# Optimization experiments

Measured on AMD Instinct MI355X. Metric: run time of the kernel, lower is better.

Reference implementation:

```python
import jax, jax.numpy as jnp
import numpy as np

P, N, E, H = 8192, 32, 256, 8
D = E // H
CUT_A, CUT_B = 0.001, 0.005  # self.length_range = (0.001, 0.005, None, None)
SQRT3 = 1.7320508075688772


def _soft_square_cutoff(x):
    # smooth ramp 0->1 on [CUT_A, CUT_B], 0 below, 1 above (high-side ranges are None)
    t = jnp.clip((x - CUT_A) / (CUT_B - CUT_A), 0.0, 1.0)
    return 0.5 * (1.0 - jnp.cos(jnp.pi * t))


def setup_inputs() -> dict:
    key = jax.random.key(0)
    ks = jax.random.split(key, 16)
    s = 1.0 / np.sqrt(E)
    inp = {
        "query": jax.random.normal(ks[0], (P, E), jnp.float32),
        "key_x": jax.random.normal(ks[1], (P, E), jnp.float32),
        "value": jax.random.normal(ks[2], (P, E), jnp.float32),
        "index_pair": jax.random.randint(ks[3], (P, N), 0, P),
        "relative_atten_weights": jax.random.normal(ks[4], (P, N, H), jnp.float32),
        # lengths ~ N(0, 0.002*sqrt(3)) so they span the (0.001, 0.005) cutoff range
        "rpe_distance": jax.random.normal(ks[5], (P, N, 3), jnp.float32) * 0.002,
        "Wq": jax.random.normal(ks[6], (E, E), jnp.float32) * s,
        "bq": jnp.zeros((E,), jnp.float32),
        "Wk": jax.random.normal(ks[7], (E, E), jnp.float32) * s,
        "bk": jnp.zeros((E,), jnp.float32),
        "Wv": jax.random.normal(ks[8], (E, E), jnp.float32) * s,
        "bv": jnp.zeros((E,), jnp.float32),
        "Wg1": jax.random.normal(ks[9], (E, 3 * H), jnp.float32) * s,
        "bg1": jnp.zeros((3 * H,), jnp.float32),
        "Wg2": jax.random.normal(ks[10], (3 * H, 3 * H), jnp.float32) * (1.0 / np.sqrt(3 * H)),
        "bg2": jnp.zeros((3 * H,), jnp.float32),
    }
    return inp


def reference(query, key_x, value, index_pair, relative_atten_weights, rpe_distance,
              Wq, bq, Wk, bk, Wv, bv, Wg1, bg1, Wg2, bg2):
    # --- RPE spherical harmonics (irreps 1x0e+1x1e, component norm); keep l=1 part ([:,1:])
    rlen = jnp.linalg.norm(rpe_distance, axis=-1, keepdims=True)        # [P,N,1]
    unit = rpe_distance / jnp.maximum(rlen, 1e-12)                      # normalize=True
    cutoff = _soft_square_cutoff(rlen)                                  # nonscalar cutoff
    rpe_edge_sh = SQRT3 * unit * cutoff                                 # [P,N,3]

    # --- projections
    q = query @ Wq + bq                                                 # [P,E]
    k = key_x @ Wk + bk
    v = value @ Wv + bv

    # --- mapper_v6: per-edge gather of key/value rows
    k_g = k[index_pair]                                                 # [P,N,E]
    v_g = v[index_pair]                                                 # [P,N,E]

    # --- dot-product attention logits
    qh = q.reshape(P, H, D)
    kh = k_g.reshape(P, N, H, D)
    dot_atten = jnp.einsum('phd,pnhd->pnh', qh, kh)                     # [P,N,H]

    # --- MLP positional bias gated by spherical harmonics
    diff = k_g - q[:, None, :]                                          # [P,N,E]
    g = jax.nn.relu(diff @ Wg1 + bg1) @ Wg2 + bg2                       # [P,N,3H]
    g = g.reshape(P, N, H, 3)
    pos_atten = jnp.sum(g * rpe_edge_sh[:, :, None, :], axis=-1)        # [P,N,H]

    atten = (dot_atten + pos_atten + relative_atten_weights) / np.sqrt(D)
    atten = jax.nn.softmax(atten, axis=1)                               # over neighbors

    vh = v_g.reshape(P, N, H, D)
    out = jnp.einsum('pnh,pnhc->phc', atten, vh).reshape(P, E)
    return out
```

## Files before the change

### kernel.cpp

```cpp
#include <hip/hip_runtime.h>
#include <stdint.h>

typedef uint32_t u32;
typedef unsigned short u16;

#define LDT 40

typedef __bf16 bf16x8 __attribute__((ext_vector_type(8)));
typedef float  f32x4  __attribute__((ext_vector_type(4)));

__device__ __forceinline__ float bf2f(u16 x) {
  union { float f; u32 u; } c; c.u = ((u32)x) << 16; return c.f;
}
__device__ __forceinline__ u16 f2bf(float f) {
  union { float f; u32 u; } c; c.f = f;
  u32 b = c.u;
  return (u16)((b + 0x7FFFu + ((b >> 16) & 1u)) >> 16);
}
__device__ __forceinline__ u32 pk2(float lo, float hi) {
  return (u32)f2bf(lo) | ((u32)f2bf(hi) << 16);
}

__global__ __launch_bounds__(256) void prep_transpose(
    const float* __restrict__ Wq, const float* __restrict__ Wk, const float* __restrict__ Wv,
    u16* __restrict__ WTq, u16* __restrict__ WTk, u16* __restrict__ WTv)
{
  int z = blockIdx.z, bx = blockIdx.x, by = blockIdx.y;
  int x = threadIdx.x, y = threadIdx.y;
  __shared__ u16 tile[32][33];
  const float* W  = (z == 0) ? Wq : (z == 1) ? Wk : Wv;
  u16*         WT = (z == 0) ? WTq : (z == 1) ? WTk : WTv;
  for (int yy = y; yy < 32; yy += 8)
    tile[yy][x] = f2bf(W[(size_t)(by * 32 + yy) * 256 + bx * 32 + x]);
  __syncthreads();
  for (int yy = y; yy < 32; yy += 8)
    WT[(size_t)(bx * 32 + yy) * 256 + by * 32 + x] = tile[x][yy];
}

__global__ __launch_bounds__(256) void prep_comb(
    const u16* __restrict__ WTq, const u16* __restrict__ WTk,
    const float* __restrict__ Wg1, const float* __restrict__ bg1,
    const float* __restrict__ bq, const float* __restrict__ bk,
    u16* __restrict__ CT, float* __restrict__ bcomb)
{
  int c = blockIdx.x, z = blockIdx.y;
  int t = threadIdx.x;
  const u16*   WT = (z == 0) ? WTq : WTk;
  const float* b  = (z == 0) ? bq : bk;

  float acc = 0.f;
#pragma unroll 8
  for (int e = 0; e < 256; e++)
    acc += bf2f(WT[(size_t)e * 256 + t]) * Wg1[(size_t)e * 24 + c];
  CT[(size_t)z * 8192 + (size_t)c * 256 + t] = f2bf(acc);

  __shared__ float red[256];
  red[t] = b[t] * Wg1[(size_t)t * 24 + c];
  __syncthreads();
  for (int s = 128; s > 0; s >>= 1) {
    if (t < s) red[t] += red[t + s];
    __syncthreads();
  }
  if (t == 0)
    bcomb[z * 24 + c] = red[0] - ((z == 0) ? bg1[c] : 0.f);
}

__global__ __launch_bounds__(256) void gemm_qkv(
    const float* __restrict__ Xq, const float* __restrict__ Xk, const float* __restrict__ Xv,
    const u16* __restrict__ WTq, const u16* __restrict__ WTk, const u16* __restrict__ WTv,
    const float* __restrict__ bq, const float* __restrict__ bk, const float* __restrict__ bv,
    const u16* __restrict__ CT, const float* __restrict__ bcomb,
    u16* __restrict__ Oq, u16* __restrict__ Ok, u16* __restrict__ Ov,
    float* __restrict__ qadj, float* __restrict__ kg1)
{
  int z = blockIdx.z;
  int nblk = blockIdx.x;
  if (nblk == 2 && z == 2) return;

  const float* X = (z == 0) ? Xq : (z == 1) ? Xk : Xv;
  int m0 = blockIdx.y * 128;
  int t = threadIdx.x;
  int lane = t & 63, wid = t >> 6;
  int fr = lane & 15, fg = lane >> 4;
  int sr = t >> 1;
  int sc = (t & 1) * 16;

  __shared__ __align__(16) u16 la[128 * LDT];
  __shared__ __align__(16) u16 lb[128 * LDT];

  if (nblk < 2) {
    const u16*   WT   = (z == 0) ? WTq : (z == 1) ? WTk : WTv;
    const float* bias = (z == 0) ? bq : (z == 1) ? bk : bv;
    u16*         O    = (z == 0) ? Oq : (z == 1) ? Ok : Ov;
    int n0 = nblk * 128;
    int wr = wid >> 1, wc = wid & 1;

    f32x4 acc[4][4];
#pragma unroll
    for (int i = 0; i < 4; i++)
#pragma unroll
      for (int j = 0; j < 4; j++) acc[i][j] = (f32x4){0.f, 0.f, 0.f, 0.f};

    for (int kt = 0; kt < 256; kt += 32) {
      const float4* ga = (const float4*)(X + (size_t)(m0 + sr) * 256 + kt + sc);
      float4 a0 = ga[0], a1 = ga[1], a2 = ga[2], a3 = ga[3];
      const uint4* gb = (const uint4*)(WT + (size_t)(n0 + sr) * 256 + kt + sc);
      uint4 b0 = gb[0], b1 = gb[1];

      uint4 wa0, wa1;
      wa0.x = pk2(a0.x, a0.y); wa0.y = pk2(a0.z, a0.w);
      wa0.z = pk2(a1.x, a1.y); wa0.w = pk2(a1.z, a1.w);
      wa1.x = pk2(a2.x, a2.y); wa1.y = pk2(a2.z, a2.w);
      wa1.z = pk2(a3.x, a3.y); wa1.w = pk2(a3.z, a3.w);

      __syncthreads();
      *(uint4*)&la[sr * LDT + sc]     = wa0;
      *(uint4*)&la[sr * LDT + sc + 8] = wa1;
      *(uint4*)&lb[sr * LDT + sc]     = b0;
      *(uint4*)&lb[sr * LDT + sc + 8] = b1;
      __syncthreads();

      bf16x8 af[4], bfr[4];
#pragma unroll
      for (int s = 0; s < 4; s++)
        af[s] = *(const bf16x8*)&la[(wr * 64 + s * 16 + fr) * LDT + fg * 8];
#pragma unroll
      for (int s = 0; s < 4; s++)
        bfr[s] = *(const bf16x8*)&lb[(wc * 64 + s * 16 + fr) * LDT + fg * 8];
#pragma unroll
      for (int i = 0; i < 4; i++)
#pragma unroll
        for (int j = 0; j < 4; j++)
          acc[i][j] = __builtin_amdgcn_mfma_f32_16x16x32_bf16(af[i], bfr[j], acc[i][j], 0, 0, 0);
    }

#pragma unroll
    for (int i = 0; i < 4; i++) {
      int rowb = m0 + wr * 64 + i * 16 + fg * 4;
#pragma unroll
      for (int j = 0; j < 4; j++) {
        int col = n0 + wc * 64 + j * 16 + fr;
        float bb = bias[col];
#pragma unroll
        for (int r = 0; r < 4; r++)
          O[(size_t)(rowb + r) * 256 + col] = f2bf(acc[i][j][r] + bb);
      }
    }
  } else {
    const u16*   BT = CT + (size_t)z * 8192;
    const float* bc = bcomb + z * 24;
    float*       O  = (z == 0) ? qadj : kg1;

    f32x4 acc[2][2];
#pragma unroll
    for (int i = 0; i < 2; i++)
#pragma unroll
      for (int j = 0; j < 2; j++) acc[i][j] = (f32x4){0.f, 0.f, 0.f, 0.f};

    for (int kt = 0; kt < 256; kt += 32) {
      const float4* ga = (const float4*)(X + (size_t)(m0 + sr) * 256 + kt + sc);
      float4 a0 = ga[0], a1 = ga[1], a2 = ga[2], a3 = ga[3];
      uint4 b0, b1;
      if (t < 64) {
        const uint4* gb = (const uint4*)(BT + (size_t)sr * 256 + kt + sc);
        b0 = gb[0]; b1 = gb[1];
      }
      uint4 wa0, wa1;
      wa0.x = pk2(a0.x, a0.y); wa0.y = pk2(a0.z, a0.w);
      wa0.z = pk2(a1.x, a1.y); wa0.w = pk2(a1.z, a1.w);
      wa1.x = pk2(a2.x, a2.y); wa1.y = pk2(a2.z, a2.w);
      wa1.z = pk2(a3.x, a3.y); wa1.w = pk2(a3.z, a3.w);

      __syncthreads();
      *(uint4*)&la[sr * LDT + sc]     = wa0;
      *(uint4*)&la[sr * LDT + sc + 8] = wa1;
      if (t < 64) {
        *(uint4*)&lb[sr * LDT + sc]     = b0;
        *(uint4*)&lb[sr * LDT + sc + 8] = b1;
      }
      __syncthreads();

      bf16x8 af[2], bfr[2];
#pragma unroll
      for (int s = 0; s < 2; s++)
        af[s] = *(const bf16x8*)&la[(wid * 32 + s * 16 + fr) * LDT + fg * 8];
#pragma unroll
      for (int s = 0; s < 2; s++)
        bfr[s] = *(const bf16x8*)&lb[(s * 16 + fr) * LDT + fg * 8];
#pragma unroll
      for (int i = 0; i < 2; i++)
#pragma unroll
        for (int j = 0; j < 2; j++)
          acc[i][j] = __builtin_amdgcn_mfma_f32_16x16x32_bf16(af[i], bfr[j], acc[i][j], 0, 0, 0);
    }

#pragma unroll
    for (int i = 0; i < 2; i++) {
      int rowb = m0 + wid * 32 + i * 16 + fg * 4;
#pragma unroll
      for (int j = 0; j < 2; j++) {
        int col = j * 16 + fr;
        if (col < 24) {
#pragma unroll
          for (int r = 0; r < 4; r++)
            O[(size_t)(rowb + r) * 24 + col] = acc[i][j][r] + bc[col];
        }
      }
    }
  }
}

__global__ __launch_bounds__(256) void attn_logits(
    const u16* __restrict__ qb, const u16* __restrict__ kb,
    const float* __restrict__ kg1, const float* __restrict__ qadj,
    const int* __restrict__ ip, const float* __restrict__ raw,
    const float* __restrict__ rpe, const float* __restrict__ wg2b,
    const float* __restrict__ bg2b, float* __restrict__ att)
{
  int p = blockIdx.x, t = threadIdx.x;
  __shared__ __align__(16) float q_s[256];
  __shared__            int   idx_s[32];
  __shared__            float rpe_s[96];
  __shared__            float sh_s[32][3];
  __shared__            float qadj_s[24];
  __shared__            float bg2_s[24];
  __shared__            float wg2_s[576];
  __shared__ __align__(16) float kg1_s[32 * 24];
  __shared__            float pre_s[32][24];
  __shared__            float logit_s[32][8];
  __shared__            float ps_s[64];
  __shared__            float is_s[8];

  q_s[t] = bf2f(qb[(size_t)p * 256 + t]);
  if (t < 96) rpe_s[t] = rpe[(size_t)p * 96 + t];
  if (t < 32) idx_s[t] = ip[(size_t)p * 32 + t];
  if (t >= 128 && t < 152) qadj_s[t - 128] = qadj[(size_t)p * 24 + (t - 128)];
  if (t >= 160 && t < 184) bg2_s[t - 160] = bg2b[t - 160];
  if (t < 192) {
    wg2_s[t]       = wg2b[t];
    wg2_s[t + 192] = wg2b[t + 192];
    wg2_s[t + 384] = wg2b[t + 384];
  }
  __syncthreads();

  if (t < 32) {
    float x  = rpe_s[t * 3 + 0];
    float y  = rpe_s[t * 3 + 1];
    float zz = rpe_s[t * 3 + 2];
    float rl = sqrtf(x * x + y * y + zz * zz);
    float inv = 1.f / fmaxf(rl, 1e-12f);
    float tt = (rl - 0.001f) * 250.f;
    tt = fminf(fmaxf(tt, 0.f), 1.f);
    float cut = 0.5f * (1.f - cosf(tt * 3.14159265358979f));
    float s3c = 1.7320508075688772f * inv * cut;
    sh_s[t][0] = x * s3c; sh_s[t][1] = y * s3c; sh_s[t][2] = zz * s3c;
  }
  if (t < 192) {
    int n = t / 6, f = t % 6;
    const float4* kp = (const float4*)(kg1 + (size_t)idx_s[n] * 24);
    *(float4*)&kg1_s[n * 24 + f * 4] = kp[f];
  }
  __syncthreads();

  {
    int n = t >> 3, jj = t & 7;
#pragma unroll
    for (int c = 0; c < 3; c++) {
      int i = jj * 3 + c;
      pre_s[n][i] = fmaxf(kg1_s[n * 24 + i] - qadj_s[i], 0.f);
    }
  }
  __syncthreads();

  {
    int n = t >> 3, h = t & 7;
    const uint4*  kr = (const uint4*)(kb + (size_t)idx_s[n] * 256 + h * 32);
    const float4* qr = (const float4*)(q_s + h * 32);
    float dot = 0.f;
#pragma unroll
    for (int c = 0; c < 4; c++) {
      uint4 kw = kr[c];
      float4 q0 = qr[2 * c], q1 = qr[2 * c + 1];
      dot += bf2f((u16)(kw.x & 0xFFFF)) * q0.x + bf2f((u16)(kw.x >> 16)) * q0.y;
      dot += bf2f((u16)(kw.y & 0xFFFF)) * q0.z + bf2f((u16)(kw.y >> 16)) * q0.w;
      dot += bf2f((u16)(kw.z & 0xFFFF)) * q1.x + bf2f((u16)(kw.z >> 16)) * q1.y;
      dot += bf2f((u16)(kw.w & 0xFFFF)) * q1.z + bf2f((u16)(kw.w >> 16)) * q1.w;
    }
    float g0 = bg2_s[h * 3 + 0], g1v = bg2_s[h * 3 + 1], g2v = bg2_s[h * 3 + 2];
#pragma unroll
    for (int i = 0; i < 24; i++) {
      float pr = pre_s[n][i];
      int b = i * 24 + h * 3;
      g0  += pr * wg2_s[b + 0];
      g1v += pr * wg2_s[b + 1];
      g2v += pr * wg2_s[b + 2];
    }
    float pos = g0 * sh_s[n][0] + g1v * sh_s[n][1] + g2v * sh_s[n][2];
    float rw = raw[(size_t)p * 256 + t];
    logit_s[n][h] = __expf((dot + pos + rw) * 0.17677669529663687f);
  }
  __syncthreads();

  if (t < 64) {
    int h = t & 7, g = t >> 3;
    float s = logit_s[g * 4 + 0][h] + logit_s[g * 4 + 1][h]
            + logit_s[g * 4 + 2][h] + logit_s[g * 4 + 3][h];
    ps_s[h * 8 + g] = s;
  }
  __syncthreads();
  if (t < 8) {
    float s = 0.f;
#pragma unroll
    for (int g = 0; g < 8; g++) s += ps_s[t * 8 + g];
    is_s[t] = 1.f / s;
  }
  __syncthreads();

  {
    int h = t >> 5, n = t & 31;
    att[(size_t)p * 256 + t] = logit_s[n][h] * is_s[h];
  }
}

__global__ __launch_bounds__(256) void attn_pv(
    const u16* __restrict__ vb, const float* __restrict__ att,
    const int* __restrict__ ip, float* __restrict__ out)
{
  int p0 = blockIdx.x * 4, t = threadIdx.x;
  int wid = t >> 6, l = t & 63;
  int p = p0 + wid;
  __shared__ __align__(16) float att_s[4][256];
  __shared__            int   idx_s[4][32];

  *(float4*)&att_s[wid][l * 4] = *(const float4*)(att + (size_t)p * 256 + l * 4);
  if (l < 32) idx_s[wid][l] = ip[(size_t)p * 32 + l];
  __syncthreads();

  int h = l >> 3;
  float a0 = 0.f, a1 = 0.f, a2 = 0.f, a3 = 0.f;
#pragma unroll
  for (int n = 0; n < 32; n++) {
    float w = att_s[wid][h * 32 + n];
    const uint2 vv = *(const uint2*)(vb + (size_t)idx_s[wid][n] * 256 + l * 4);
    a0 += w * bf2f((u16)(vv.x & 0xFFFF));
    a1 += w * bf2f((u16)(vv.x >> 16));
    a2 += w * bf2f((u16)(vv.y & 0xFFFF));
    a3 += w * bf2f((u16)(vv.y >> 16));
  }
  float4 r; r.x = a0; r.y = a1; r.z = a2; r.w = a3;
  *(float4*)(out + (size_t)p * 256 + l * 4) = r;
}

extern "C" void kernel_launch(void* const* d_in, const int* in_sizes, int n_in,
                              void* d_out, int out_size, void* d_ws, size_t ws_size,
                              hipStream_t stream) {
  const float* query = (const float*)d_in[0];
  const float* key_x = (const float*)d_in[1];
  const float* value = (const float*)d_in[2];
  const int*   index_pair = (const int*)d_in[3];
  const float* raw  = (const float*)d_in[4];
  const float* rpe  = (const float*)d_in[5];
  const float* Wq = (const float*)d_in[6];
  const float* bq = (const float*)d_in[7];
  const float* Wk = (const float*)d_in[8];
  const float* bk = (const float*)d_in[9];
  const float* Wv = (const float*)d_in[10];
  const float* bv = (const float*)d_in[11];
  const float* Wg1 = (const float*)d_in[12];
  const float* bg1 = (const float*)d_in[13];
  const float* Wg2 = (const float*)d_in[14];
  const float* bg2 = (const float*)d_in[15];
  float* out = (float*)d_out;

  char* ws = (char*)d_ws;
  u16*   qbuf = (u16*)(ws);
  u16*   kbuf = (u16*)(ws + (4u << 20));
  u16*   vbuf = (u16*)(ws + (8u << 20));
  float* att  = (float*)(ws + (12u << 20));
  float* qadj = (float*)(ws + (20u << 20));
  float* kg1  = (float*)(ws + (20u << 20) + 786432);
  u16*   WTq  = (u16*)(ws + (20u << 20) + 2 * 786432);
  u16*   WTk  = WTq + 65536;
  u16*   WTv  = WTk + 65536;
  u16*   CT   = WTv + 65536;
  float* bcomb = (float*)(CT + 16384);

  prep_transpose<<<dim3(8, 8, 3), dim3(32, 8, 1), 0, stream>>>(
      Wq, Wk, Wv, WTq, WTk, WTv);
  prep_comb<<<dim3(24, 2), 256, 0, stream>>>(
      WTq, WTk, Wg1, bg1, bq, bk, CT, bcomb);
  gemm_qkv<<<dim3(3, 64, 3), 256, 0, stream>>>(
      query, key_x, value, WTq, WTk, WTv, bq, bk, bv, CT, bcomb,
      qbuf, kbuf, vbuf, qadj, kg1);
  attn_logits<<<8192, 256, 0, stream>>>(
      qbuf, kbuf, kg1, qadj, index_pair, raw, rpe, Wg2, bg2, att);
  attn_pv<<<2048, 256, 0, stream>>>(
      vbuf, att, index_pair, out);
}
```

Baseline: 79.12 us.

## Fuse attention logits and PV into one kernel; use MFMA for gate MLP

```diff
diff --git a/kernel.cpp b/kernel.cpp
--- a/kernel.cpp
+++ b/kernel.cpp
@@ -210,39 +210,50 @@
   }
 }
 
-__global__ __launch_bounds__(256) void attn_logits(
-    const u16* __restrict__ qb, const u16* __restrict__ kb,
+__global__ __launch_bounds__(256) void edge_attn(
+    const u16* __restrict__ qb, const u16* __restrict__ kb, const u16* __restrict__ vb,
     const float* __restrict__ kg1, const float* __restrict__ qadj,
     const int* __restrict__ ip, const float* __restrict__ raw,
-    const float* __restrict__ rpe, const float* __restrict__ wg2b,
-    const float* __restrict__ bg2b, float* __restrict__ att)
+    const float* __restrict__ rpe, const float* __restrict__ wg2g,
+    const float* __restrict__ bg2g, float* __restrict__ out)
 {
   int p = blockIdx.x, t = threadIdx.x;
+  int lane = t & 63, w = t >> 6;
+
   __shared__ __align__(16) float q_s[256];
-  __shared__            int   idx_s[32];
-  __shared__            float rpe_s[96];
-  __shared__            float sh_s[32][3];
-  __shared__            float qadj_s[24];
-  __shared__            float bg2_s[24];
-  __shared__            float wg2_s[576];
+  __shared__              int   idx_s[32];
+  __shared__              float rpe_s[96];
+  __shared__              float sh_s[32][3];
+  __shared__              float qadj_s[24];
+  __shared__              float bg2_s[24];
+  __shared__ __align__(16) u16  wg2T[32 * 40];
+  __shared__ __align__(16) u16  preb[32 * 40];
   __shared__ __align__(16) float kg1_s[32 * 24];
-  __shared__            float pre_s[32][24];
-  __shared__            float logit_s[32][8];
-  __shared__            float ps_s[64];
-  __shared__            float is_s[8];
+  __shared__              float g_s[32 * 33];
+  __shared__              float logit_s[32][8];
+  __shared__              float ps_s[64];
+  __shared__              float is_s[8];
+  __shared__ __align__(16) float pv_s[4 * 256];
 
   q_s[t] = bf2f(qb[(size_t)p * 256 + t]);
+  if (t < 32) idx_s[t] = ip[(size_t)p * 32 + t];
   if (t < 96) rpe_s[t] = rpe[(size_t)p * 96 + t];
-  if (t < 32) idx_s[t] = ip[(size_t)p * 32 + t];
   if (t >= 128 && t < 152) qadj_s[t - 128] = qadj[(size_t)p * 24 + (t - 128)];
-  if (t >= 160 && t < 184) bg2_s[t - 160] = bg2b[t - 160];
+  if (t >= 160 && t < 184) bg2_s[t - 160] = bg2g[t - 160];
+  {
+    int s0 = 2 * t, s1 = 2 * t + 1;
+    { int i = s0 / 24, j = s0 - i * 24; if (s0 < 576) wg2T[j * 40 + i] = f2bf(wg2g[s0]); }
+    { int i = s1 / 24, j = s1 - i * 24; if (s1 < 576) wg2T[j * 40 + i] = f2bf(wg2g[s1]); }
+    if (t < 64) { int s = 512 + t; int i = s / 24, j = s - i * 24; wg2T[j * 40 + i] = f2bf(wg2g[s]); }
+    wg2T[(t >> 3) * 40 + 24 + (t & 7)] = 0;
+    if (t < 192) wg2T[(24 + t / 24) * 40 + (t % 24)] = 0;
+  }
+  __syncthreads();
+
   if (t < 192) {
-    wg2_s[t]       = wg2b[t];
-    wg2_s[t + 192] = wg2b[t + 192];
-    wg2_s[t + 384] = wg2b[t + 384];
-  }
-  __syncthreads();
-
+    int n = t / 6, f = t % 6;
+    *(float4*)&kg1_s[n * 24 + f * 4] = ((const float4*)(kg1 + (size_t)idx_s[n] * 24))[f];
+  }
   if (t < 32) {
     float x  = rpe_s[t * 3 + 0];
     float y  = rpe_s[t * 3 + 1];
@@ -255,20 +266,34 @@
     float s3c = 1.7320508075688772f * inv * cut;
     sh_s[t][0] = x * s3c; sh_s[t][1] = y * s3c; sh_s[t][2] = zz * s3c;
   }
-  if (t < 192) {
-    int n = t / 6, f = t % 6;
-    const float4* kp = (const float4*)(kg1 + (size_t)idx_s[n] * 24);
-    *(float4*)&kg1_s[n * 24 + f * 4] = kp[f];
-  }
   __syncthreads();
 
   {
     int n = t >> 3, jj = t & 7;
-#pragma unroll
-    for (int c = 0; c < 3; c++) {
-      int i = jj * 3 + c;
-      pre_s[n][i] = fmaxf(kg1_s[n * 24 + i] - qadj_s[i], 0.f);
-    }
+    float v0, v1, v2, v3;
+    int j0 = jj * 4;
+    v0 = (j0 + 0 < 24) ? fmaxf(kg1_s[n * 24 + j0 + 0] - qadj_s[j0 + 0], 0.f) : 0.f;
+    v1 = (j0 + 1 < 24) ? fmaxf(kg1_s[n * 24 + j0 + 1] - qadj_s[j0 + 1], 0.f) : 0.f;
+    v2 = (j0 + 2 < 24) ? fmaxf(kg1_s[n * 24 + j0 + 2] - qadj_s[j0 + 2], 0.f) : 0.f;
+    v3 = (j0 + 3 < 24) ? fmaxf(kg1_s[n * 24 + j0 + 3] - qadj_s[j0 + 3], 0.f) : 0.f;
+    uint2 pw; pw.x = pk2(v0, v1); pw.y = pk2(v2, v3);
+    *(uint2*)&preb[n * 40 + j0] = pw;
+  }
+  __syncthreads();
+
+  {
+    int mt = w & 1, nt = w >> 1;
+    int fr = lane & 15, fg = lane >> 4;
+    bf16x8 a = *(const bf16x8*)&preb[(mt * 16 + fr) * 40 + fg * 8];
+    bf16x8 b = *(const bf16x8*)&wg2T[(nt * 16 + fr) * 40 + fg * 8];
+    f32x4 acc = (f32x4){0.f, 0.f, 0.f, 0.f};
+    acc = __builtin_amdgcn_mfma_f32_16x16x32_bf16(a, b, acc, 0, 0, 0);
+    int j = nt * 16 + fr;
+    float bb = (j < 24) ? bg2_s[j] : 0.f;
+    int e0 = mt * 16 + fg * 4;
+#pragma unroll
+    for (int r = 0; r < 4; r++)
+      g_s[(e0 + r) * 33 + j] = acc[r] + bb;
   }
   __syncthreads();
 
@@ -286,16 +311,9 @@
       dot += bf2f((u16)(kw.z & 0xFFFF)) * q1.x + bf2f((u16)(kw.z >> 16)) * q1.y;
       dot += bf2f((u16)(kw.w & 0xFFFF)) * q1.z + bf2f((u16)(kw.w >> 16)) * q1.w;
     }
-    float g0 = bg2_s[h * 3 + 0], g1v = bg2_s[h * 3 + 1], g2v = bg2_s[h * 3 + 2];
-#pragma unroll
-    for (int i = 0; i < 24; i++) {
-      float pr = pre_s[n][i];
-      int b = i * 24 + h * 3;
-      g0  += pr * wg2_s[b + 0];
-      g1v += pr * wg2_s[b + 1];
-      g2v += pr * wg2_s[b + 2];
-    }
-    float pos = g0 * sh_s[n][0] + g1v * sh_s[n][1] + g2v * sh_s[n][2];
+    float pos = g_s[n * 33 + h * 3 + 0] * sh_s[n][0]
+              + g_s[n * 33 + h * 3 + 1] * sh_s[n][1]
+              + g_s[n * 33 + h * 3 + 2] * sh_s[n][2];
     float rw = raw[(size_t)p * 256 + t];
     logit_s[n][h] = __expf((dot + pos + rw) * 0.17677669529663687f);
   }
@@ -303,9 +321,8 @@
 
   if (t < 64) {
     int h = t & 7, g = t >> 3;
-    float s = logit_s[g * 4 + 0][h] + logit_s[g * 4 + 1][h]
-            + logit_s[g * 4 + 2][h] + logit_s[g * 4 + 3][h];
-    ps_s[h * 8 + g] = s;
+    ps_s[h * 8 + g] = logit_s[g * 4 + 0][h] + logit_s[g * 4 + 1][h]
+                    + logit_s[g * 4 + 2][h] + logit_s[g * 4 + 3][h];
   }
   __syncthreads();
   if (t < 8) {
@@ -317,38 +334,26 @@
   __syncthreads();
 
   {
-    int h = t >> 5, n = t & 31;
-    att[(size_t)p * 256 + t] = logit_s[n][h] * is_s[h];
-  }
-}
-
-__global__ __launch_bounds__(256) void attn_pv(
-    const u16* __restrict__ vb, const float* __restrict__ att,
-    const int* __restrict__ ip, float* __restrict__ out)
-{
-  int p0 = blockIdx.x * 4, t = threadIdx.x;
-  int wid = t >> 6, l = t & 63;
-  int p = p0 + wid;
-  __shared__ __align__(16) float att_s[4][256];
-  __shared__            int   idx_s[4][32];
-
-  *(float4*)&att_s[wid][l * 4] = *(const float4*)(att + (size_t)p * 256 + l * 4);
-  if (l < 32) idx_s[wid][l] = ip[(size_t)p * 32 + l];
-  __syncthreads();
-
-  int h = l >> 3;
-  float a0 = 0.f, a1 = 0.f, a2 = 0.f, a3 = 0.f;
-#pragma unroll
-  for (int n = 0; n < 32; n++) {
-    float w = att_s[wid][h * 32 + n];
-    const uint2 vv = *(const uint2*)(vb + (size_t)idx_s[wid][n] * 256 + l * 4);
-    a0 += w * bf2f((u16)(vv.x & 0xFFFF));
-    a1 += w * bf2f((u16)(vv.x >> 16));
-    a2 += w * bf2f((u16)(vv.y & 0xFFFF));
-    a3 += w * bf2f((u16)(vv.y >> 16));
-  }
-  float4 r; r.x = a0; r.y = a1; r.z = a2; r.w = a3;
-  *(float4*)(out + (size_t)p * 256 + l * 4) = r;
+    int c0 = lane * 4;
+    int hh = lane >> 3;
+    float isv = is_s[hh];
+    float a0 = 0.f, a1 = 0.f, a2 = 0.f, a3 = 0.f;
+#pragma unroll
+    for (int i = 0; i < 8; i++) {
+      int n = w * 8 + i;
+      float wt = logit_s[n][hh] * isv;
+      uint2 vv = *(const uint2*)(vb + (size_t)idx_s[n] * 256 + c0);
+      a0 += wt * bf2f((u16)(vv.x & 0xFFFF));
+      a1 += wt * bf2f((u16)(vv.x >> 16));
+      a2 += wt * bf2f((u16)(vv.y & 0xFFFF));
+      a3 += wt * bf2f((u16)(vv.y >> 16));
+    }
+    float4 r; r.x = a0; r.y = a1; r.z = a2; r.w = a3;
+    *(float4*)&pv_s[w * 256 + c0] = r;
+  }
+  __syncthreads();
+
+  out[(size_t)p * 256 + t] = pv_s[t] + pv_s[256 + t] + pv_s[512 + t] + pv_s[768 + t];
 }
 
 extern "C" void kernel_launch(void* const* d_in, const int* in_sizes, int n_in,
@@ -376,10 +381,9 @@
   u16*   qbuf = (u16*)(ws);
   u16*   kbuf = (u16*)(ws + (4u << 20));
   u16*   vbuf = (u16*)(ws + (8u << 20));
-  float* att  = (float*)(ws + (12u << 20));
-  float* qadj = (float*)(ws + (20u << 20));
-  float* kg1  = (float*)(ws + (20u << 20) + 786432);
-  u16*   WTq  = (u16*)(ws + (20u << 20) + 2 * 786432);
+  float* qadj = (float*)(ws + (12u << 20));
+  float* kg1  = (float*)(ws + (12u << 20) + 786432);
+  u16*   WTq  = (u16*)(ws + (12u << 20) + 2 * 786432);
   u16*   WTk  = WTq + 65536;
   u16*   WTv  = WTk + 65536;
   u16*   CT   = WTv + 65536;
@@ -392,8 +396,6 @@
   gemm_qkv<<<dim3(3, 64, 3), 256, 0, stream>>>(
       query, key_x, value, WTq, WTk, WTv, bq, bk, bv, CT, bcomb,
       qbuf, kbuf, vbuf, qadj, kg1);
-  attn_logits<<<8192, 256, 0, stream>>>(
-      qbuf, kbuf, kg1, qadj, index_pair, raw, rpe, Wg2, bg2, att);
-  attn_pv<<<2048, 256, 0, stream>>>(
-      vbuf, att, index_pair, out);
-}
+  edge_attn<<<8192, 256, 0, stream>>>(
+      qbuf, kbuf, vbuf, kg1, qadj, index_pair, raw, rpe, Wg2, bg2, out);
+}
```

New measurement: 75.69 us. 4.3% less time.
